# Kernel optimization log

Hardware: AMD Instinct MI355X
Metric: run time of the kernel (lower is better)

## Reference

```python
import jax, jax.numpy as jnp
import numpy as np

B, C, CI, H, W = 4, 64, 32, 64, 64
EPS = 1e-5


def _bn(x, gamma, beta, mean, var):
    # inference-mode BatchNorm2d; x: [B,C,H,W], params: [C]
    scale = gamma / jnp.sqrt(var + EPS)
    return (x - mean[:, None, None]) * scale[:, None, None] + beta[:, None, None]


def _conv1x1(x, w, b):
    # 1x1 conv == channel matmul; w: [Cout,Cin], b: [Cout]
    return jnp.einsum('bchw,oc->bohw', x, w) + b[:, None, None]


def setup_inputs() -> dict:
    key = jax.random.key(0)
    ks = jax.random.split(key, 32)
    nrm = lambda k, shape, s=0.05: jax.random.normal(k, shape, jnp.float32) * s
    inp = {
        'x1': jax.random.normal(ks[0], (B, C, H, W), jnp.float32),
        'x2': jax.random.normal(ks[1], (B, C, H, W), jnp.float32),
    }
    i = 2
    for name, (cin, cout, bn_c) in [('g', (C, CI, C)), ('th', (C, CI, C)), ('ph', (C, CI, C)), ('w', (CI, C, C))]:
        inp[f'{name}_w'] = nrm(ks[i], (cout, cin), 0.1); i += 1
        inp[f'{name}_b'] = nrm(ks[i], (cout,)); i += 1
        inp[f'{name}_gamma'] = 1.0 + nrm(ks[i], (bn_c,)); i += 1
        inp[f'{name}_beta'] = nrm(ks[i], (bn_c,)); i += 1
        inp[f'{name}_mean'] = nrm(ks[i], (bn_c,)); i += 1
        inp[f'{name}_var'] = 1.0 + 0.1 * jax.random.uniform(ks[i], (bn_c,), jnp.float32); i += 1
    return inp


def reference(x1, x2,
              g_w, g_b, g_gamma, g_beta, g_mean, g_var,
              th_w, th_b, th_gamma, th_beta, th_mean, th_var,
              ph_w, ph_b, ph_gamma, ph_beta, ph_mean, ph_var,
              w_w, w_b, w_gamma, w_beta, w_mean, w_var):
    b, c, h, w = x1.shape
    n = h * w

    def proj(x, cw, cb, ga, be, mu, va):  # BN -> 1x1 conv -> flatten spatial
        return _conv1x1(_bn(x, ga, be, mu, va), cw, cb).reshape(b, CI, n)

    def out_proj(y):  # 1x1 conv -> BN (the W block)
        return _bn(_conv1x1(y, w_w, w_b), w_gamma, w_beta, w_mean, w_var)

    g1 = proj(x1, g_w, g_b, g_gamma, g_beta, g_mean, g_var)      # [B,CI,N]
    g2 = proj(x2, g_w, g_b, g_gamma, g_beta, g_mean, g_var)      # [B,CI,N]
    th1 = proj(x1, th_w, th_b, th_gamma, th_beta, th_mean, th_var)  # theta(x1) [B,CI,N]
    ph2 = proj(x2, ph_w, ph_b, ph_gamma, ph_beta, ph_mean, ph_var)  # phi(x2)   [B,CI,N]

    energy = jnp.einsum('bcn,bcm->bnm', th1, ph2)  # theta^T @ phi, [B,N,N]
    attention = jax.nn.softmax(energy, axis=-2)    # softmax over dim=-2 as in torch

    y1 = jnp.einsum('bcn,bnm->bcm', g1, attention).reshape(b, CI, h, w)
    y2 = jnp.einsum('bcm,bnm->bcn', g2, attention).reshape(b, CI, h, w)

    return (x1 + out_proj(y1), x2 + out_proj(y2))
```

## Files before the change

### kernel.cpp

```cpp
#include <hip/hip_runtime.h>
#include <math.h>

#define BB 4
#define CC 64
#define CI 32
#define NN 4096
#define EPS 1e-5f

#define PROJ_SZ (BB * CI * NN)

typedef __attribute__((ext_vector_type(8))) short bf16x8;
typedef __attribute__((ext_vector_type(4))) float f32x4;

__device__ __forceinline__ ushort f2bf(float f) {
    uint u = __builtin_bit_cast(uint, f);
    u += 0x7FFFu + ((u >> 16) & 1u);
    return (ushort)(u >> 16);
}
__device__ __forceinline__ float bf2f(ushort h) {
    uint u = (uint)h << 16;
    return __builtin_bit_cast(float, u);
}
__device__ __forceinline__ uint pk2(float a, float b) {
    uint r;
    asm("v_cvt_pk_bf16_f32 %0, %1, %2" : "=v"(r) : "v"(a), "v"(b));
    return r;
}
__device__ __forceinline__ bf16x8 mk8(uint a, uint b, uint c, uint d) {
    uint4 u; u.x = a; u.y = b; u.z = c; u.w = d;
    return __builtin_bit_cast(bf16x8, u);
}
__device__ __forceinline__ int inv_pi(int r) {
    return 8 * ((r & 15) >> 2) + (r & 3) + 4 * (r >> 4);
}

__global__ __launch_bounds__(256) void proj_kernel(
    const float* __restrict__ x1, const float* __restrict__ x2,
    const float* __restrict__ gw, const float* __restrict__ gb,
    const float* __restrict__ gga, const float* __restrict__ gbe,
    const float* __restrict__ gmu, const float* __restrict__ gva,
    const float* __restrict__ tw, const float* __restrict__ tb,
    const float* __restrict__ tga, const float* __restrict__ tbe,
    const float* __restrict__ tmu, const float* __restrict__ tva,
    const float* __restrict__ pw, const float* __restrict__ pb,
    const float* __restrict__ pga, const float* __restrict__ pbe,
    const float* __restrict__ pmu, const float* __restrict__ pva,
    ushort* __restrict__ g1p, ushort* __restrict__ g2o,
    ushort* __restrict__ thTo, ushort* __restrict__ phTo)
{
    int job = blockIdx.y;
    const float* src = (job == 0 || job == 2) ? x1 : x2;
    const float *w, *bia, *ga, *be, *mu, *va;
    if (job <= 1)      { w = gw; bia = gb; ga = gga; be = gbe; mu = gmu; va = gva; }
    else if (job == 2) { w = tw; bia = tb; ga = tga; be = tbe; mu = tmu; va = tva; }
    else               { w = pw; bia = pb; ga = pga; be = pbe; mu = pmu; va = pva; }

    __shared__ __align__(16) float s_w[CI][CC];
    __shared__ float s_scale[CC], s_shift[CC], s_b[CI];
    int t = threadIdx.x;
    if (t < CC) {
        float sc = ga[t] / sqrtf(va[t] + EPS);
        s_scale[t] = sc;
        s_shift[t] = be[t] - mu[t] * sc;
    }
    if (t >= CC && t < CC + CI) s_b[t - CC] = bia[t - CC];
    for (int i = t; i < CI * CC; i += 256) s_w[i / CC][i % CC] = w[i];
    __syncthreads();

    int bn = blockIdx.x * 256 + t;
    int b = bn >> 12, n = bn & (NN - 1);
    const float* xp = src + ((size_t)b * CC) * NN + n;

    float acc[CI];
#pragma unroll
    for (int o = 0; o < CI; o++) acc[o] = s_b[o];

#pragma unroll 4
    for (int c4 = 0; c4 < CC / 4; c4++) {
        float xv0 = xp[(size_t)(c4 * 4 + 0) * NN] * s_scale[c4 * 4 + 0] + s_shift[c4 * 4 + 0];
        float xv1 = xp[(size_t)(c4 * 4 + 1) * NN] * s_scale[c4 * 4 + 1] + s_shift[c4 * 4 + 1];
        float xv2 = xp[(size_t)(c4 * 4 + 2) * NN] * s_scale[c4 * 4 + 2] + s_shift[c4 * 4 + 2];
        float xv3 = xp[(size_t)(c4 * 4 + 3) * NN] * s_scale[c4 * 4 + 3] + s_shift[c4 * 4 + 3];
#pragma unroll
        for (int o = 0; o < CI; o++) {
            float4 wv = *(const float4*)&s_w[o][c4 * 4];
            acc[o] += wv.x * xv0 + wv.y * xv1 + wv.z * xv2 + wv.w * xv3;
        }
    }

    if (job == 0) {
        int nb = n >> 5, pos = inv_pi(n & 31);
        ushort* dp = g1p + (((size_t)b * 128 + nb) * 32) * 32 + pos;
#pragma unroll
        for (int o = 0; o < CI; o++) dp[o * 32] = f2bf(acc[o]);
    } else if (job == 1) {
        ushort* dp = g2o + ((size_t)b * CI) * NN + n;
#pragma unroll
        for (int o = 0; o < CI; o++) dp[(size_t)o * NN] = f2bf(acc[o]);
    } else {
        if (job == 2) {
#pragma unroll
            for (int o = 0; o < CI; o++) acc[o] *= 1.44269504f;
        }
        uint u[16];
#pragma unroll
        for (int i = 0; i < 16; i++)
            u[i] = (uint)f2bf(acc[2 * i]) | ((uint)f2bf(acc[2 * i + 1]) << 16);
        uint4* dp = (uint4*)((job == 2 ? thTo : phTo) + ((size_t)b * NN + n) * CI);
#pragma unroll
        for (int i = 0; i < 4; i++) {
            uint4 v; v.x = u[4 * i]; v.y = u[4 * i + 1]; v.z = u[4 * i + 2]; v.w = u[4 * i + 3];
            dp[i] = v;
        }
    }
}

__global__ __launch_bounds__(256, 8) void passA_kernel(
    const ushort* __restrict__ thT, const ushort* __restrict__ phT,
    const ushort* __restrict__ g1p,
    float* __restrict__ zpart, float* __restrict__ y1part, int NCH)
{
    const int t = threadIdx.x;
    const int wave = t >> 6, lane = t & 63;
    const int q = lane >> 4, lm = lane & 15;
    const int b = blockIdx.y, ch = blockIdx.z;
    const int m0 = blockIdx.x * 64;
    const int m = m0 + wave * 16 + lm;
    const size_t bN = (size_t)b * NN;

    const bf16x8 bS = *(const bf16x8*)(phT + (bN + m) * CI + 8 * q);

    f32x4 acc0 = {0.f, 0.f, 0.f, 0.f};
    f32x4 acc1 = {0.f, 0.f, 0.f, 0.f};
    const f32x4 z4 = {0.f, 0.f, 0.f, 0.f};
    float zacc = 0.f;

    const int nchunk = NN / NCH;
    const int nbeg = ch * nchunk;
    const ushort* ta = thT + (bN + nbeg + lm) * CI + 8 * q;
    const ushort* gp = g1p + (((size_t)b * 128 + (nbeg >> 5)) * 32 + lm) * 32 + 8 * q;

    for (int it = 0; it < nchunk / 64; it++) {
        bf16x8 a0 = *(const bf16x8*)(ta);
        bf16x8 a1 = *(const bf16x8*)(ta + 16 * CI);
        bf16x8 a2 = *(const bf16x8*)(ta + 32 * CI);
        bf16x8 a3 = *(const bf16x8*)(ta + 48 * CI);
        bf16x8 ga00 = *(const bf16x8*)(gp);
        bf16x8 ga10 = *(const bf16x8*)(gp + 512);
        bf16x8 ga01 = *(const bf16x8*)(gp + 1024);
        bf16x8 ga11 = *(const bf16x8*)(gp + 1536);

        f32x4 d0 = __builtin_amdgcn_mfma_f32_16x16x32_bf16(a0, bS, z4, 0, 0, 0);
        f32x4 d1 = __builtin_amdgcn_mfma_f32_16x16x32_bf16(a1, bS, z4, 0, 0, 0);
        f32x4 d2 = __builtin_amdgcn_mfma_f32_16x16x32_bf16(a2, bS, z4, 0, 0, 0);
        f32x4 d3 = __builtin_amdgcn_mfma_f32_16x16x32_bf16(a3, bS, z4, 0, 0, 0);

        f32x4 p0, p1, p2, p3;
#pragma unroll
        for (int r = 0; r < 4; r++) {
            p0[r] = __builtin_amdgcn_exp2f(d0[r]);
            p1[r] = __builtin_amdgcn_exp2f(d1[r]);
            p2[r] = __builtin_amdgcn_exp2f(d2[r]);
            p3[r] = __builtin_amdgcn_exp2f(d3[r]);
        }
        zacc += ((p0[0] + p0[1]) + (p0[2] + p0[3]))
              + ((p1[0] + p1[1]) + (p1[2] + p1[3]))
              + ((p2[0] + p2[1]) + (p2[2] + p2[3]))
              + ((p3[0] + p3[1]) + (p3[2] + p3[3]));

        bf16x8 bP0 = mk8(pk2(p0[0], p0[1]), pk2(p0[2], p0[3]),
                         pk2(p1[0], p1[1]), pk2(p1[2], p1[3]));
        bf16x8 bP1 = mk8(pk2(p2[0], p2[1]), pk2(p2[2], p2[3]),
                         pk2(p3[0], p3[1]), pk2(p3[2], p3[3]));

        acc0 = __builtin_amdgcn_mfma_f32_16x16x32_bf16(ga00, bP0, acc0, 0, 0, 0);
        acc0 = __builtin_amdgcn_mfma_f32_16x16x32_bf16(ga01, bP1, acc0, 0, 0, 0);
        acc1 = __builtin_amdgcn_mfma_f32_16x16x32_bf16(ga10, bP0, acc1, 0, 0, 0);
        acc1 = __builtin_amdgcn_mfma_f32_16x16x32_bf16(ga11, bP1, acc1, 0, 0, 0);

        ta += 64 * CI;
        gp += 2048;
    }

    zacc += __shfl_xor(zacc, 16);
    zacc += __shfl_xor(zacc, 32);
    if (q == 0) zpart[((size_t)ch * BB + b) * NN + m] = zacc;

    float* yp = y1part + (((size_t)ch * BB + b) * CI) * NN + m;
#pragma unroll
    for (int r = 0; r < 4; r++) {
        yp[(size_t)(4 * q + r) * NN] = acc0[r];
        yp[(size_t)(16 + 4 * q + r) * NN] = acc1[r];
    }
}

__global__ __launch_bounds__(256) void combine_kernel(
    const float* __restrict__ zpart, const ushort* __restrict__ g2,
    float* __restrict__ rZ, ushort* __restrict__ g2s, int NCH)
{
    int idx = blockIdx.x * 256 + threadIdx.x;
    float z = 0.f;
    for (int ch = 0; ch < NCH; ch++) z += zpart[(size_t)ch * BB * NN + idx];
    float r = 1.f / z;
    rZ[idx] = r;
    int b = idx >> 12, mm = idx & (NN - 1);
    int mb = mm >> 5, pos = inv_pi(mm & 31);
    const ushort* gpi = g2 + (size_t)b * CI * NN + mm;
    ushort* gso = g2s + (((size_t)b * 128 + mb) * 32) * 32 + pos;
#pragma unroll
    for (int c = 0; c < CI; c++) gso[c * 32] = f2bf(bf2f(gpi[(size_t)c * NN]) * r);
}

__global__ __launch_bounds__(256, 8) void passB_kernel(
    const ushort* __restrict__ thT, const ushort* __restrict__ phT,
    const ushort* __restrict__ g2s,
    float* __restrict__ y2part, int NCH)
{
    const int t = threadIdx.x;
    const int wave = t >> 6, lane = t & 63;
    const int q = lane >> 4, lm = lane & 15;
    const int b = blockIdx.y, ch = blockIdx.z;
    const int n0 = blockIdx.x * 64;
    const int n = n0 + wave * 16 + lm;
    const size_t bN = (size_t)b * NN;

    const bf16x8 bT = *(const bf16x8*)(thT + (bN + n) * CI + 8 * q);

    f32x4 acc0 = {0.f, 0.f, 0.f, 0.f};
    f32x4 acc1 = {0.f, 0.f, 0.f, 0.f};
    const f32x4 z4 = {0.f, 0.f, 0.f, 0.f};

    const int mchunk = NN / NCH;
    const int mbeg = ch * mchunk;
    const ushort* pa = phT + (bN + mbeg + lm) * CI + 8 * q;
    const ushort* gp = g2s + (((size_t)b * 128 + (mbeg >> 5)) * 32 + lm) * 32 + 8 * q;

    for (int it = 0; it < mchunk / 64; it++) {
        bf16x8 a0 = *(const bf16x8*)(pa);
        bf16x8 a1 = *(const bf16x8*)(pa + 16 * CI);
        bf16x8 a2 = *(const bf16x8*)(pa + 32 * CI);
        bf16x8 a3 = *(const bf16x8*)(pa + 48 * CI);
        bf16x8 ga00 = *(const bf16x8*)(gp);
        bf16x8 ga10 = *(const bf16x8*)(gp + 512);
        bf16x8 ga01 = *(const bf16x8*)(gp + 1024);
        bf16x8 ga11 = *(const bf16x8*)(gp + 1536);

        f32x4 d0 = __builtin_amdgcn_mfma_f32_16x16x32_bf16(a0, bT, z4, 0, 0, 0);
        f32x4 d1 = __builtin_amdgcn_mfma_f32_16x16x32_bf16(a1, bT, z4, 0, 0, 0);
        f32x4 d2 = __builtin_amdgcn_mfma_f32_16x16x32_bf16(a2, bT, z4, 0, 0, 0);
        f32x4 d3 = __builtin_amdgcn_mfma_f32_16x16x32_bf16(a3, bT, z4, 0, 0, 0);

        f32x4 p0, p1, p2, p3;
#pragma unroll
        for (int r = 0; r < 4; r++) {
            p0[r] = __builtin_amdgcn_exp2f(d0[r]);
            p1[r] = __builtin_amdgcn_exp2f(d1[r]);
            p2[r] = __builtin_amdgcn_exp2f(d2[r]);
            p3[r] = __builtin_amdgcn_exp2f(d3[r]);
        }

        bf16x8 bP0 = mk8(pk2(p0[0], p0[1]), pk2(p0[2], p0[3]),
                         pk2(p1[0], p1[1]), pk2(p1[2], p1[3]));
        bf16x8 bP1 = mk8(pk2(p2[0], p2[1]), pk2(p2[2], p2[3]),
                         pk2(p3[0], p3[1]), pk2(p3[2], p3[3]));

        acc0 = __builtin_amdgcn_mfma_f32_16x16x32_bf16(ga00, bP0, acc0, 0, 0, 0);
        acc0 = __builtin_amdgcn_mfma_f32_16x16x32_bf16(ga01, bP1, acc0, 0, 0, 0);
        acc1 = __builtin_amdgcn_mfma_f32_16x16x32_bf16(ga10, bP0, acc1, 0, 0, 0);
        acc1 = __builtin_amdgcn_mfma_f32_16x16x32_bf16(ga11, bP1, acc1, 0, 0, 0);

        pa += 64 * CI;
        gp += 2048;
    }

    float* yp = y2part + (((size_t)ch * BB + b) * CI) * NN + n;
#pragma unroll
    for (int r = 0; r < 4; r++) {
        yp[(size_t)(4 * q + r) * NN] = acc0[r];
        yp[(size_t)(16 + 4 * q + r) * NN] = acc1[r];
    }
}

__global__ __launch_bounds__(256) void final_kernel(
    const float* __restrict__ x1, const float* __restrict__ x2,
    const float* __restrict__ ww, const float* __restrict__ wb,
    const float* __restrict__ wga, const float* __restrict__ wbe,
    const float* __restrict__ wmu, const float* __restrict__ wva,
    const float* __restrict__ y1part, const float* __restrict__ y2part,
    const float* __restrict__ rZ, float* __restrict__ out, int NCH)
{
    int job = blockIdx.y;
    const float* part = job ? y2part : y1part;
    const float* x = job ? x2 : x1;
    float* o = out + (size_t)job * (BB * CC * NN);

    __shared__ __align__(16) float s_w[CC][CI];
    __shared__ float s_scale[CC], s_bias[CC];
    int t = threadIdx.x;
    if (t < CC) {
        float sc = wga[t] / sqrtf(wva[t] + EPS);
        s_scale[t] = sc;
        s_bias[t] = wbe[t] - wmu[t] * sc + wb[t] * sc;
    }
    __syncthreads();
    for (int i = t; i < CC * CI; i += 256) s_w[i / CI][i % CI] = ww[i] * s_scale[i / CI];
    __syncthreads();

    int idx = blockIdx.x * 256 + t;
    int b = idx >> 12, j = idx & (NN - 1);

    float y[CI];
#pragma unroll
    for (int c = 0; c < CI; c++) y[c] = 0.f;
    for (int ch = 0; ch < NCH; ch++) {
        const float* pp = part + (((size_t)ch * BB + b) * CI) * NN + j;
#pragma unroll
        for (int c = 0; c < CI; c++) y[c] += pp[(size_t)c * NN];
    }
    if (job == 0) {
        float r = rZ[idx];
#pragma unroll
        for (int c = 0; c < CI; c++) y[c] *= r;
    }

    const float* xp = x + ((size_t)b * CC) * NN + j;
    float* op = o + ((size_t)b * CC) * NN + j;
#pragma unroll
    for (int oo = 0; oo < CC; oo++) {
        float acc = s_bias[oo];
        const float4* wr = (const float4*)s_w[oo];
#pragma unroll
        for (int c4 = 0; c4 < CI / 4; c4++) {
            float4 wv = wr[c4];
            acc += wv.x * y[c4 * 4] + wv.y * y[c4 * 4 + 1] + wv.z * y[c4 * 4 + 2] + wv.w * y[c4 * 4 + 3];
        }
        op[(size_t)oo * NN] = xp[(size_t)oo * NN] + acc;
    }
}

extern "C" void kernel_launch(void* const* d_in, const int* in_sizes, int n_in,
                              void* d_out, int out_size, void* d_ws, size_t ws_size,
                              hipStream_t stream)
{
    const float* x1  = (const float*)d_in[0];
    const float* x2  = (const float*)d_in[1];
    const float* gw  = (const float*)d_in[2];
    const float* gb  = (const float*)d_in[3];
    const float* gga = (const float*)d_in[4];
    const float* gbe = (const float*)d_in[5];
    const float* gmu = (const float*)d_in[6];
    const float* gva = (const float*)d_in[7];
    const float* tw  = (const float*)d_in[8];
    const float* tb  = (const float*)d_in[9];
    const float* tga = (const float*)d_in[10];
    const float* tbe = (const float*)d_in[11];
    const float* tmu = (const float*)d_in[12];
    const float* tva = (const float*)d_in[13];
    const float* pw  = (const float*)d_in[14];
    const float* pb  = (const float*)d_in[15];
    const float* pga = (const float*)d_in[16];
    const float* pbe = (const float*)d_in[17];
    const float* pmu = (const float*)d_in[18];
    const float* pva = (const float*)d_in[19];
    const float* ww  = (const float*)d_in[20];
    const float* wb  = (const float*)d_in[21];
    const float* wga = (const float*)d_in[22];
    const float* wbe = (const float*)d_in[23];
    const float* wmu = (const float*)d_in[24];
    const float* wva = (const float*)d_in[25];

    int NC = 8;
    while (NC > 1) {
        size_t need = 5ull * PROJ_SZ * 2
                    + (size_t)NC * BB * NN * 4
                    + (size_t)BB * NN * 4
                    + 2ull * NC * BB * CI * NN * 4;
        if (need <= ws_size) break;
        NC >>= 1;
    }

    ushort* g1p  = (ushort*)d_ws;
    ushort* g2   = g1p + PROJ_SZ;
    ushort* g2s  = g2 + PROJ_SZ;
    ushort* thT  = g2s + PROJ_SZ;
    ushort* phT  = thT + PROJ_SZ;
    float* zpart = (float*)(phT + PROJ_SZ);
    float* rZ    = zpart + (size_t)NC * BB * NN;
    float* y1p   = rZ + (size_t)BB * NN;
    float* y2p   = y1p + (size_t)NC * BB * CI * NN;

    proj_kernel<<<dim3(BB * NN / 256, 4), 256, 0, stream>>>(
        x1, x2, gw, gb, gga, gbe, gmu, gva, tw, tb, tga, tbe, tmu, tva,
        pw, pb, pga, pbe, pmu, pva, g1p, g2, thT, phT);

    passA_kernel<<<dim3(NN / 64, BB, NC), 256, 0, stream>>>(
        thT, phT, g1p, zpart, y1p, NC);

    combine_kernel<<<dim3(BB * NN / 256), 256, 0, stream>>>(
        zpart, g2, rZ, g2s, NC);

    passB_kernel<<<dim3(NN / 64, BB, NC), 256, 0, stream>>>(
        thT, phT, g2s, y2p, NC);

    final_kernel<<<dim3(BB * NN / 256, 2), 256, 0, stream>>>(
        x1, x2, ww, wb, wga, wbe, wmu, wva, y1p, y2p, rZ, (float*)d_out, NC);
}
```

Before: 249.1 us.

## Split combine and final kernels into finer-grained parallel stages

The combine kernel is split into a 1/Z reduction kernel and a separate per-element g2 scaling kernel with far more threads. The final kernel is split into a vectorized float4 reduction over chunk partials and an epilogue kernel that handles 16 output channels per block slice. The goal is more parallelism and occupancy for the small, latency-bound tail stages. In exchange it adds two kernel launches and extra global round trips through new y1r/y2r buffers, and the scale kernel's scattered writes may be poorly coalesced.

Result: faster. 218.7 us (-12.2%).

```diff
diff --git a/kernel.cpp b/kernel.cpp
--- a/kernel.cpp
+++ b/kernel.cpp
@@ -194,21 +194,27 @@
     }
 }
 
-__global__ __launch_bounds__(256) void combine_kernel(
-    const float* __restrict__ zpart, const ushort* __restrict__ g2,
-    float* __restrict__ rZ, ushort* __restrict__ g2s, int NCH)
+__global__ __launch_bounds__(256) void rz_kernel(
+    const float* __restrict__ zpart, float* __restrict__ rZ, int NCH)
 {
     int idx = blockIdx.x * 256 + threadIdx.x;
     float z = 0.f;
     for (int ch = 0; ch < NCH; ch++) z += zpart[(size_t)ch * BB * NN + idx];
-    float r = 1.f / z;
-    rZ[idx] = r;
-    int b = idx >> 12, mm = idx & (NN - 1);
-    int mb = mm >> 5, pos = inv_pi(mm & 31);
-    const ushort* gpi = g2 + (size_t)b * CI * NN + mm;
-    ushort* gso = g2s + (((size_t)b * 128 + mb) * 32) * 32 + pos;
-#pragma unroll
-    for (int c = 0; c < CI; c++) gso[c * 32] = f2bf(bf2f(gpi[(size_t)c * NN]) * r);
+    rZ[idx] = 1.f / z;
+}
+
+__global__ __launch_bounds__(256) void scale_g2_kernel(
+    const ushort* __restrict__ g2, const float* __restrict__ rZ,
+    ushort* __restrict__ g2s)
+{
+    int id = blockIdx.x * 256 + threadIdx.x;
+    int b = id >> 17;
+    int rem = id & ((1 << 17) - 1);
+    int c = rem >> 12;
+    int m = rem & (NN - 1);
+    float v = bf2f(g2[(size_t)b * CI * NN + (size_t)c * NN + m]) * rZ[b * NN + m];
+    int mb = m >> 5, pos = inv_pi(m & 31);
+    g2s[(((size_t)b * 128 + mb) * 32 + c) * 32 + pos] = f2bf(v);
 }
 
 __global__ __launch_bounds__(256, 8) void passB_kernel(
@@ -281,60 +287,83 @@
     }
 }
 
-__global__ __launch_bounds__(256) void final_kernel(
+__global__ __launch_bounds__(256) void reduce_kernel(
+    const float* __restrict__ y1p, const float* __restrict__ y2p,
+    const float* __restrict__ rZ,
+    float* __restrict__ y1r, float* __restrict__ y2r, int NCH)
+{
+    int id = blockIdx.x * 256 + threadIdx.x;
+    int job = id >> 17;
+    int f4 = id & ((1 << 17) - 1);
+    int b = f4 >> 15;
+    int rem = f4 & ((1 << 15) - 1);
+    int c = rem >> 10;
+    int j4 = rem & 1023;
+
+    const float* part = job ? y2p : y1p;
+    size_t off = ((size_t)b * CI + c) * NN + (size_t)j4 * 4;
+    float4 s = {0.f, 0.f, 0.f, 0.f};
+    for (int ch = 0; ch < NCH; ch++) {
+        float4 v = *(const float4*)(part + (size_t)ch * BB * CI * NN + off);
+        s.x += v.x; s.y += v.y; s.z += v.z; s.w += v.w;
+    }
+    if (job == 0) {
+        float4 r = *(const float4*)(rZ + (size_t)b * NN + (size_t)j4 * 4);
+        s.x *= r.x; s.y *= r.y; s.z *= r.z; s.w *= r.w;
+    }
+    *(float4*)((job ? y2r : y1r) + off) = s;
+}
+
+__global__ __launch_bounds__(256) void epilogue_kernel(
     const float* __restrict__ x1, const float* __restrict__ x2,
     const float* __restrict__ ww, const float* __restrict__ wb,
     const float* __restrict__ wga, const float* __restrict__ wbe,
     const float* __restrict__ wmu, const float* __restrict__ wva,
-    const float* __restrict__ y1part, const float* __restrict__ y2part,
-    const float* __restrict__ rZ, float* __restrict__ out, int NCH)
+    const float* __restrict__ y1r, const float* __restrict__ y2r,
+    float* __restrict__ out)
 {
     int job = blockIdx.y;
-    const float* part = job ? y2part : y1part;
+    int slice = blockIdx.z;
+    const float* yr = job ? y2r : y1r;
     const float* x = job ? x2 : x1;
     float* o = out + (size_t)job * (BB * CC * NN);
 
-    __shared__ __align__(16) float s_w[CC][CI];
-    __shared__ float s_scale[CC], s_bias[CC];
+    __shared__ __align__(16) float s_w[16][CI];
+    __shared__ float s_bias[16];
     int t = threadIdx.x;
-    if (t < CC) {
-        float sc = wga[t] / sqrtf(wva[t] + EPS);
-        s_scale[t] = sc;
-        s_bias[t] = wbe[t] - wmu[t] * sc + wb[t] * sc;
-    }
-    __syncthreads();
-    for (int i = t; i < CC * CI; i += 256) s_w[i / CI][i % CI] = ww[i] * s_scale[i / CI];
+    if (t < 16) {
+        int oo = slice * 16 + t;
+        float sc = wga[oo] / sqrtf(wva[oo] + EPS);
+        s_bias[t] = wbe[oo] - wmu[oo] * sc + wb[oo] * sc;
+    }
+    for (int i = t; i < 16 * CI; i += 256) {
+        int k = i / CI, c = i % CI;
+        int oo = slice * 16 + k;
+        float sc = wga[oo] / sqrtf(wva[oo] + EPS);
+        s_w[k][c] = ww[oo * CI + c] * sc;
+    }
     __syncthreads();
 
     int idx = blockIdx.x * 256 + t;
     int b = idx >> 12, j = idx & (NN - 1);
 
     float y[CI];
-#pragma unroll
-    for (int c = 0; c < CI; c++) y[c] = 0.f;
-    for (int ch = 0; ch < NCH; ch++) {
-        const float* pp = part + (((size_t)ch * BB + b) * CI) * NN + j;
-#pragma unroll
-        for (int c = 0; c < CI; c++) y[c] += pp[(size_t)c * NN];
-    }
-    if (job == 0) {
-        float r = rZ[idx];
-#pragma unroll
-        for (int c = 0; c < CI; c++) y[c] *= r;
-    }
-
-    const float* xp = x + ((size_t)b * CC) * NN + j;
-    float* op = o + ((size_t)b * CC) * NN + j;
-#pragma unroll
-    for (int oo = 0; oo < CC; oo++) {
-        float acc = s_bias[oo];
-        const float4* wr = (const float4*)s_w[oo];
+    const float* yp = yr + ((size_t)b * CI) * NN + j;
+#pragma unroll
+    for (int c = 0; c < CI; c++) y[c] = yp[(size_t)c * NN];
+
+    const float* xp = x + ((size_t)b * CC + slice * 16) * NN + j;
+    float* op = o + ((size_t)b * CC + slice * 16) * NN + j;
+#pragma unroll
+    for (int k = 0; k < 16; k++) {
+        float acc = s_bias[k];
 #pragma unroll
         for (int c4 = 0; c4 < CI / 4; c4++) {
-            float4 wv = wr[c4];
-            acc += wv.x * y[c4 * 4] + wv.y * y[c4 * 4 + 1] + wv.z * y[c4 * 4 + 2] + wv.w * y[c4 * 4 + 3];
-        }
-        op[(size_t)oo * NN] = xp[(size_t)oo * NN] + acc;
+            float4 wv = *(const float4*)&s_w[k][c4 * 4];
+            acc += wv.x * y[c4 * 4] + wv.y * y[c4 * 4 + 1]
+                 + wv.z * y[c4 * 4 + 2] + wv.w * y[c4 * 4 + 3];
+        }
+        op[(size_t)k * NN] = xp[(size_t)k * NN] + acc;
     }
 }
 
@@ -374,7 +403,8 @@
         size_t need = 5ull * PROJ_SZ * 2
                     + (size_t)NC * BB * NN * 4
                     + (size_t)BB * NN * 4
-                    + 2ull * NC * BB * CI * NN * 4;
+                    + 2ull * NC * BB * CI * NN * 4
+                    + 2ull * BB * CI * NN * 4;
         if (need <= ws_size) break;
         NC >>= 1;
     }
@@ -388,6 +418,8 @@
     float* rZ    = zpart + (size_t)NC * BB * NN;
     float* y1p   = rZ + (size_t)BB * NN;
     float* y2p   = y1p + (size_t)NC * BB * CI * NN;
+    float* y1r   = y2p + (size_t)NC * BB * CI * NN;
+    float* y2r   = y1r + (size_t)BB * CI * NN;
 
     proj_kernel<<<dim3(BB * NN / 256, 4), 256, 0, stream>>>(
         x1, x2, gw, gb, gga, gbe, gmu, gva, tw, tb, tga, tbe, tmu, tva,
@@ -396,12 +428,16 @@
     passA_kernel<<<dim3(NN / 64, BB, NC), 256, 0, stream>>>(
         thT, phT, g1p, zpart, y1p, NC);
 
-    combine_kernel<<<dim3(BB * NN / 256), 256, 0, stream>>>(
-        zpart, g2, rZ, g2s, NC);
+    rz_kernel<<<dim3(BB * NN / 256), 256, 0, stream>>>(zpart, rZ, NC);
+
+    scale_g2_kernel<<<dim3(BB * CI * NN / 256), 256, 0, stream>>>(g2, rZ, g2s);
 
     passB_kernel<<<dim3(NN / 64, BB, NC), 256, 0, stream>>>(
         thT, phT, g2s, y2p, NC);
 
-    final_kernel<<<dim3(BB * NN / 256, 2), 256, 0, stream>>>(
-        x1, x2, ww, wb, wga, wbe, wmu, wva, y1p, y2p, rZ, (float*)d_out, NC);
-}
+    reduce_kernel<<<dim3(2 * BB * CI * NN / 4 / 256), 256, 0, stream>>>(
+        y1p, y2p, rZ, y1r, y2r, NC);
+
+    epilogue_kernel<<<dim3(BB * NN / 256, 2, 4), 256, 0, stream>>>(
+        x1, x2, ww, wb, wga, wbe, wmu, wva, y1r, y2r, (float*)d_out);
+}
```
